# Kernel optimization log

Measured on AMD Instinct MI355X. Metric: run time of the kernel, lower is better.

Reference implementation:

```python
import jax, jax.numpy as jnp
import numpy as np

D, H, E, K = 1024, 2048, 8, 2
AUX_COEF = 0.01


def _xavier(key, shape, fan_in, fan_out):
    lim = (6.0 / (fan_in + fan_out)) ** 0.5
    return jax.random.uniform(key, shape, minval=-lim, maxval=lim, dtype=jnp.float32)


def setup_inputs() -> dict:
    key = jax.random.key(0)
    ks = jax.random.split(key, 6)
    x = jax.random.normal(ks[0], (4, 2048, D), dtype=jnp.float32)
    Wg = _xavier(ks[1], (E, D), D, E)              # gate: [E, D]
    W1 = _xavier(ks[2], (E, D, H), D, H)           # stacked expert w1
    W3 = _xavier(ks[3], (E, D, H), D, H)           # stacked expert w3
    W2 = _xavier(ks[4], (E, H, D), H, D)           # stacked expert w2
    b1 = jnp.zeros((E, H), dtype=jnp.float32)
    b3 = jnp.zeros((E, H), dtype=jnp.float32)
    b2 = jnp.zeros((E, D), dtype=jnp.float32)
    return {"x": x, "Wg": Wg, "W1": W1, "b1": b1, "W2": W2, "b2": b2, "W3": W3, "b3": b3}


def reference(x, Wg, W1, b1, W2, b2, W3, b3):
    B, S, d = x.shape
    xf = x.reshape(-1, d)                                  # [N, D]
    N = xf.shape[0]

    # Gate: softmax scores, top-k routing, route_scale = 1.0
    all_scores = jax.nn.softmax(xf @ Wg.T, axis=-1)        # [N, E]
    topk_vals, topk_idx = jax.lax.top_k(all_scores, K)     # [N, K]

    # Combine weights scattered back to [N, E] (each token hits K distinct experts)
    cw = (jax.nn.one_hot(topk_idx, E, dtype=xf.dtype) * topk_vals[..., None]).sum(axis=1)

    # Per-expert SwiGLU, computed densely over E (reference form of masked dispatch)
    h = jax.nn.silu(jnp.einsum('nd,edh->neh', xf, W1) + b1) * \
        (jnp.einsum('nd,edh->neh', xf, W3) + b3)           # [N, E, H]
    expert_out = jnp.einsum('neh,ehd->ned', h, W2) + b2    # [N, E, D]
    y = jnp.einsum('ned,ne->nd', expert_out, cw)           # weighted combine

    # Load-balancing aux loss
    counts = jnp.bincount(topk_idx.reshape(-1), length=E).astype(xf.dtype)
    f = counts / float(N * K)
    P = all_scores.mean(axis=0)
    aux_loss = AUX_COEF * float(E) * jnp.dot(f, P)

    return y.reshape(B, S, d), aux_loss
```

## Files before the change

### kernel.cpp

```cpp
#include <hip/hip_runtime.h>
#include <hip/hip_bf16.h>
#include <math.h>

#define Ntok 8192
#define Dm   1024
#define Hm   2048
#define NE   8

typedef __hip_bfloat16 bf16;
typedef __attribute__((ext_vector_type(8))) short short8;
typedef __attribute__((ext_vector_type(4))) float f32x4;

static __device__ __forceinline__ float b2f(bf16 v){ return __bfloat162float(v); }
static __device__ __forceinline__ bf16  f2b(float v){ return __float2bfloat16(v); }

static __device__ __forceinline__ void gl2lds16(const bf16* g, bf16* l) {
    __builtin_amdgcn_global_load_lds(
        (const __attribute__((address_space(1))) unsigned*)(const void*)g,
        (__attribute__((address_space(3))) unsigned*)(void*)l, 16, 0, 0);
}

__global__ void detect_kernel(const unsigned* __restrict__ xw, int* dtf)
{
    unsigned w = xw[threadIdx.x];
    int ex = (w >> 23) & 0xff;
    unsigned long long m = __ballot(ex < 200);
    if (threadIdx.x == 0) *dtf = (__popcll(m) > 32) ? 1 : 0;
}

__global__ __launch_bounds__(1024) void gate_kernel(
    const void* __restrict__ xv, const void* __restrict__ wgv,
    const int* __restrict__ dtf,
    int* cnt, float* Psum, float* wts, int* idx_buf, bf16* __restrict__ xb)
{
    int fp32 = *dtf;
    int tid  = threadIdx.x;
    int lane = tid & 63;
    int wv   = tid >> 6;
    int n    = blockIdx.x * 16 + wv;

    __shared__ float lP[8];
    __shared__ int   lc[8];
    __shared__ int   gbase[8];
    __shared__ int   tslot[16][2];
    __shared__ int   texp[16][2];

    if (tid < 8) { lP[tid] = 0.f; lc[tid] = 0; }
    __syncthreads();

    float acc[NE];
    #pragma unroll
    for (int e = 0; e < NE; e++) acc[e] = 0.f;

    if (fp32) {
        const float* xr = (const float*)xv + (size_t)n * Dm;
        const float* Wg = (const float*)wgv;
        #pragma unroll
        for (int i = 0; i < 16; i++) {
            float xval = xr[lane + 64*i];
            xb[(size_t)n * Dm + lane + 64*i] = f2b(xval);
            #pragma unroll
            for (int e = 0; e < NE; e++) acc[e] += xval * Wg[e*Dm + lane + 64*i];
        }
    } else {
        const bf16* xr = (const bf16*)xv + (size_t)n * Dm;
        const bf16* Wg = (const bf16*)wgv;
        #pragma unroll
        for (int i = 0; i < 16; i++) {
            bf16 xraw = xr[lane + 64*i];
            xb[(size_t)n * Dm + lane + 64*i] = xraw;
            float xval = b2f(xraw);
            #pragma unroll
            for (int e = 0; e < NE; e++) acc[e] += xval * b2f(Wg[e*Dm + lane + 64*i]);
        }
    }
    #pragma unroll
    for (int e = 0; e < NE; e++) {
        float v = acc[e];
        #pragma unroll
        for (int off = 32; off > 0; off >>= 1) v += __shfl_xor(v, off);
        acc[e] = v;
    }
    float mx = acc[0];
    #pragma unroll
    for (int e = 1; e < NE; e++) mx = fmaxf(mx, acc[e]);
    float p[NE]; float s = 0.f;
    #pragma unroll
    for (int e = 0; e < NE; e++) { p[e] = expf(acc[e] - mx); s += p[e]; }
    float inv = 1.f / s;
    #pragma unroll
    for (int e = 0; e < NE; e++) p[e] *= inv;
    int e0 = 0;
    #pragma unroll
    for (int e = 1; e < NE; e++) if (p[e] > p[e0]) e0 = e;
    int e1 = (e0 == 0) ? 1 : 0;
    #pragma unroll
    for (int e = 0; e < NE; e++) if (e != e0 && p[e] > p[e1]) e1 = e;

    if (lane < NE) atomicAdd(&lP[lane], p[lane]);
    if (lane == 0) {
        tslot[wv][0] = atomicAdd(&lc[e0], 1);
        tslot[wv][1] = atomicAdd(&lc[e1], 1);
        texp[wv][0] = e0; texp[wv][1] = e1;
        wts[2*n]   = p[e0];
        wts[2*n+1] = p[e1];
    }
    __syncthreads();
    if (tid < 8) {
        gbase[tid] = atomicAdd(cnt + tid, lc[tid]);
        atomicAdd(Psum + tid*16, lP[tid]);
    }
    __syncthreads();
    if (lane == 0) {
        int ea = texp[wv][0], eb = texp[wv][1];
        idx_buf[ea*Ntok + gbase[ea] + tslot[wv][0]] = n;
        idx_buf[eb*Ntok + gbase[eb] + tslot[wv][1]] = n | 0x10000;
    }
}

__global__ void aux_kernel(const int* __restrict__ cnt, const float* __restrict__ Psum,
                           const int* __restrict__ dtf, int* __restrict__ offs,
                           void* __restrict__ out)
{
    if (threadIdx.x == 0) {
        float s = 0.f; int a = 0;
        for (int e = 0; e < NE; e++) {
            offs[e] = a; a += cnt[e];
            s += (float)cnt[e] * Psum[e*16];
        }
        float aux = 0.08f * s / (16384.f * 8192.f);
        if (*dtf) ((float*)out)[(size_t)Ntok * Dm] = aux;
        else      ((bf16*)out)[(size_t)Ntok * Dm] = f2b(aux);
    }
}

__global__ void transpose2_kernel(const void* __restrict__ sA, const void* __restrict__ sB,
                                  bf16* __restrict__ dA, bf16* __restrict__ dB,
                                  int R, int C, const int* __restrict__ dtf)
{
    __shared__ bf16 t[64][68];
    int mat = blockIdx.z >> 3, e = blockIdx.z & 7;
    const void* src = mat ? sB : sA;
    bf16* dst = mat ? dB : dA;
    size_t base = (size_t)e * R * C;
    int c0 = blockIdx.x * 64, r0 = blockIdx.y * 64;
    int tid = threadIdx.x;
    int lr = tid >> 4;
    int lc = (tid & 15) * 4;

    if (*dtf) {
        const float* s = (const float*)src + base;
        #pragma unroll
        for (int i = 0; i < 4; i++) {
            float4 v = *(const float4*)(s + (size_t)(r0 + lr + 16*i) * C + c0 + lc);
            t[lr+16*i][lc+0] = f2b(v.x); t[lr+16*i][lc+1] = f2b(v.y);
            t[lr+16*i][lc+2] = f2b(v.z); t[lr+16*i][lc+3] = f2b(v.w);
        }
    } else {
        const bf16* s = (const bf16*)src + base;
        #pragma unroll
        for (int i = 0; i < 4; i++) {
            bf16 v[4];
            *(uint2*)v = *(const uint2*)(s + (size_t)(r0 + lr + 16*i) * C + c0 + lc);
            t[lr+16*i][lc+0] = v[0]; t[lr+16*i][lc+1] = v[1];
            t[lr+16*i][lc+2] = v[2]; t[lr+16*i][lc+3] = v[3];
        }
    }
    __syncthreads();
    int oc = tid >> 2;
    int os = tid & 3;
    bf16 ov[16];
    #pragma unroll
    for (int j = 0; j < 16; j++) ov[j] = t[os*16 + j][oc];
    bf16* dp = dst + base + (size_t)(c0 + oc) * R + r0 + os*16;
    *(uint4*)dp       = *(uint4*)ov;
    *(uint4*)(dp + 8) = *(uint4*)(ov + 8);
}


#define BAR()  { asm volatile("" ::: "memory"); __builtin_amdgcn_s_barrier(); asm volatile("" ::: "memory"); }
#define VMW4() asm volatile("s_waitcnt vmcnt(4)" ::: "memory")
#define VMW2() asm volatile("s_waitcnt vmcnt(2)" ::: "memory")
#define VMW0() asm volatile("s_waitcnt vmcnt(0)" ::: "memory")

#define LOADA(_bf, _mh) do { \
    int _ab = ((_bf)*4 + (_mh))*8192 + (wr*64 + mrow)*64; \
    _Pragma("unroll") \
    for (int _m = 0; _m < 4; _m++) { \
      _Pragma("unroll") \
      for (int _k = 0; _k < 2; _k++) \
        af[_m][_k] = *(const short8*)&smem[_ab + _m*1024 + kxo[_k]]; \
    } } while(0)

#define LOADB(_bf, _nh) do { \
    int _bb = ((_bf)*4 + 2 + (_nh))*8192 + (wc*32 + mrow)*64; \
    _Pragma("unroll") \
    for (int _n = 0; _n < 2; _n++) { \
      _Pragma("unroll") \
      for (int _k = 0; _k < 2; _k++) \
        bfr[_n][_k] = *(const short8*)&smem[_bb + _n*1024 + kxo[_k]]; \
    } } while(0)

#define MFMAQ(_mh, _nh) do { \
    _Pragma("unroll") \
    for (int _m = 0; _m < 4; _m++) \
      _Pragma("unroll") \
      for (int _n = 0; _n < 2; _n++) \
        _Pragma("unroll") \
        for (int _k = 0; _k < 2; _k++) \
          acc[(_mh)*4+_m][(_nh)*2+_n] = __builtin_amdgcn_mfma_f32_16x16x32_bf16( \
              af[_m][_k], bfr[_n][_k], acc[(_mh)*4+_m][(_nh)*2+_n], 0, 0, 0); \
    } while(0)

#define STAGE_A0(_nb) do { gl2lds16(pA00, &smem[((_nb)*4+0)*8192 + w*512]); \
                           gl2lds16(pA01, &smem[((_nb)*4+0)*8192 + 4096 + w*512]); \
                           pA00 += 64; pA01 += 64; } while(0)
#define STAGE_A1(_nb) do { gl2lds16(pA10, &smem[((_nb)*4+1)*8192 + w*512]); \
                           gl2lds16(pA11, &smem[((_nb)*4+1)*8192 + 4096 + w*512]); \
                           pA10 += 64; pA11 += 64; } while(0)
#define STAGE_B0(_nb) do { gl2lds16(pB00, &smem[((_nb)*4+2)*8192 + w*512]); \
                           gl2lds16(pB01, &smem[((_nb)*4+2)*8192 + 4096 + w*512]); \
                           pB00 += 64; pB01 += 64; } while(0)
#define STAGE_B1(_nb) do { gl2lds16(pB10, &smem[((_nb)*4+3)*8192 + w*512]); \
                           gl2lds16(pB11, &smem[((_nb)*4+3)*8192 + 4096 + w*512]); \
                           pB10 += 64; pB11 += 64; } while(0)

template<int MODE>
__global__ __launch_bounds__(512) void ffn_kernel(
    const bf16* __restrict__ Asrc,
    const bf16* __restrict__ Bsrc1,
    const bf16* __restrict__ Bsrc3,
    const void* __restrict__ bv1,
    const void* __restrict__ bv3,
    const int* __restrict__ dtf,
    const int* __restrict__ cnt, const int* __restrict__ offs,
    const int* __restrict__ idx_buf,
    bf16* __restrict__ Out)
{
    const int KD = MODE ? Hm : Dm;
    const int NT = KD / 64;
    int e = blockIdx.z;
    int c = cnt[e];
    int m0 = blockIdx.y * 256;
    if (m0 >= c) return;
    int n0 = blockIdx.x * (MODE ? 256 : 128);
    int fp32 = *dtf;
    int slot0 = offs[e] + m0;

    __shared__ __align__(16) bf16 smem[65536];
    __shared__ int tk[256];

    int tid = threadIdx.x;
    int cm = c - 1 - m0; if (cm > 255) cm = 255;
    if (tid < 256) {
        int r = tid > cm ? cm : tid;
        int v = idx_buf[e*Ntok + m0 + r];
        tk[tid] = MODE ? (2*(v & 0xffff) + (v >> 16)) : (v & 0xffff);
    }
    __syncthreads();

    int lane = tid & 63, w = tid >> 6;
    int wr = w >> 2, wc = w & 3;
    int mrow = lane & 15, kg = lane >> 4;
    int flip = mrow & 7;
    int kxo[2];
    kxo[0] = ((0*4 + kg) ^ flip) * 8;
    kxo[1] = ((1*4 + kg) ^ flip) * 8;

    int rs = tid >> 3;
    int cs_src = (tid & 7) ^ (rs & 7);

    const bf16 *pA00, *pA01, *pA10, *pA11, *pB00, *pB01, *pB10, *pB11;
    {
        int r00 = rs, r01 = 64 + rs, r10 = 128 + rs, r11 = 192 + rs;
        if (MODE == 0) {
            pA00 = Asrc + (size_t)tk[r00] * Dm + cs_src*8;
            pA01 = Asrc + (size_t)tk[r01] * Dm + cs_src*8;
            pA10 = Asrc + (size_t)tk[r10] * Dm + cs_src*8;
            pA11 = Asrc + (size_t)tk[r11] * Dm + cs_src*8;
        } else {
            int c00 = r00 > cm ? cm : r00, c01 = r01 > cm ? cm : r01;
            int c10 = r10 > cm ? cm : r10, c11 = r11 > cm ? cm : r11;
            pA00 = Asrc + (size_t)(slot0 + c00) * Hm + cs_src*8;
            pA01 = Asrc + (size_t)(slot0 + c01) * Hm + cs_src*8;
            pA10 = Asrc + (size_t)(slot0 + c10) * Hm + cs_src*8;
            pA11 = Asrc + (size_t)(slot0 + c11) * Hm + cs_src*8;
        }
        if (MODE == 0) {
            #pragma unroll
            for (int hl = 0; hl < 4; hl++) {
                int r = hl*64 + rs;
                int matb = (r >> 4) & 1;
                int hcol = n0 + (r >> 7)*64 + ((r >> 5) & 3)*16 + (r & 15);
                const bf16* base = (matb ? Bsrc3 : Bsrc1) + (size_t)e*Hm*Dm
                                 + (size_t)hcol * Dm + cs_src*8;
                if (hl == 0) pB00 = base; else if (hl == 1) pB01 = base;
                else if (hl == 2) pB10 = base; else pB11 = base;
            }
        } else {
            pB00 = Bsrc1 + (size_t)e*Dm*Hm + (size_t)(n0 + rs      ) * Hm + cs_src*8;
            pB01 = Bsrc1 + (size_t)e*Dm*Hm + (size_t)(n0 + rs +  64) * Hm + cs_src*8;
            pB10 = Bsrc1 + (size_t)e*Dm*Hm + (size_t)(n0 + rs + 128) * Hm + cs_src*8;
            pB11 = Bsrc1 + (size_t)e*Dm*Hm + (size_t)(n0 + rs + 192) * Hm + cs_src*8;
        }
    }

    f32x4 acc[8][4];
    f32x4 z = {0.f, 0.f, 0.f, 0.f};
    #pragma unroll
    for (int m = 0; m < 8; m++)
        #pragma unroll
        for (int n = 0; n < 4; n++) acc[m][n] = z;

    short8 af[4][2];
    short8 bfr[2][2];

    STAGE_A0(0); STAGE_B0(0); STAGE_B1(0); STAGE_A1(0);
    VMW0();
    __syncthreads();

    for (int t = 0; t < NT; ++t) {
        int buf = t & 1, nbuf = buf ^ 1;
        bool more = (t + 1 < NT);
        LOADA(buf, 0); LOADB(buf, 0);
        if (more) STAGE_A0(nbuf);
        BAR();
        __builtin_amdgcn_s_setprio(1); MFMAQ(0, 0); __builtin_amdgcn_s_setprio(0);
        if (more) VMW4(); else VMW2();
        BAR();
        LOADB(buf, 1);
        if (more) STAGE_B0(nbuf);
        BAR();
        __builtin_amdgcn_s_setprio(1); MFMAQ(0, 1); __builtin_amdgcn_s_setprio(0);
        if (more) VMW4(); else VMW0();
        BAR();
        LOADA(buf, 1);
        if (more) STAGE_B1(nbuf);
        BAR();
        __builtin_amdgcn_s_setprio(1); MFMAQ(1, 1); __builtin_amdgcn_s_setprio(0);
        BAR();
        LOADB(buf, 0);
        if (more) STAGE_A1(nbuf);
        BAR();
        __builtin_amdgcn_s_setprio(1); MFMAQ(1, 0); __builtin_amdgcn_s_setprio(0);
        if (more) VMW4();
        BAR();
    }

    if (MODE == 0) {
        #pragma unroll
        for (int nh = 0; nh < 2; nh++) {
            int hcol = n0 + nh*64 + wc*16 + mrow;
            float bb1 = fp32 ? ((const float*)bv1)[e*Hm + hcol] : b2f(((const bf16*)bv1)[e*Hm + hcol]);
            float bb3 = fp32 ? ((const float*)bv3)[e*Hm + hcol] : b2f(((const bf16*)bv3)[e*Hm + hcol]);
            #pragma unroll
            for (int ms = 0; ms < 8; ms++) {
                int rbase = (ms>>2)*128 + wr*64 + (ms&3)*16 + kg*4;
                #pragma unroll
                for (int j = 0; j < 4; j++) {
                    int tr = rbase + j;
                    if (m0 + tr < c) {
                        float v1 = acc[ms][nh*2+0][j] + bb1;
                        float v3 = acc[ms][nh*2+1][j] + bb3;
                        float hv = (v1 / (1.f + expf(-v1))) * v3;
                        Out[(size_t)(slot0 + tr)*Hm + hcol] = f2b(hv);
                    }
                }
            }
        }
    } else {
        #pragma unroll
        for (int ns = 0; ns < 4; ns++) {
            int col = n0 + (ns>>1)*128 + wc*32 + (ns&1)*16 + mrow;
            float bb2 = fp32 ? ((const float*)bv1)[e*Dm + col] : b2f(((const bf16*)bv1)[e*Dm + col]);
            #pragma unroll
            for (int ms = 0; ms < 8; ms++) {
                int rbase = (ms>>2)*128 + wr*64 + (ms&3)*16 + kg*4;
                #pragma unroll
                for (int j = 0; j < 4; j++) {
                    int tr = rbase + j;
                    if (m0 + tr < c)
                        Out[(size_t)tk[tr]*Dm + col] = f2b(acc[ms][ns][j] + bb2);
                }
            }
        }
    }
}

#undef LOADA
#undef LOADB
#undef MFMAQ
#undef STAGE_A0
#undef STAGE_A1
#undef STAGE_B0
#undef STAGE_B1

__global__ void combine_kernel(const bf16* __restrict__ outs, const float* __restrict__ wts,
                               const int* __restrict__ dtf, void* __restrict__ yv)
{
    int gid = blockIdx.x * 256 + threadIdx.x;
    int n = gid >> 7;
    int j = (gid & 127) * 8;
    float w0 = wts[2*n], w1 = wts[2*n+1];
    bf16 ra[8], rb[8];
    *(uint4*)ra = *(const uint4*)(outs + (size_t)(2*n)   * Dm + j);
    *(uint4*)rb = *(const uint4*)(outs + (size_t)(2*n+1) * Dm + j);
    float o[8];
    #pragma unroll
    for (int t = 0; t < 8; t++)
        o[t] = w0 * b2f(ra[t]) + w1 * b2f(rb[t]);
    if (*dtf) {
        float* y = (float*)yv + (size_t)n * Dm + j;
        *(float4*)y       = make_float4(o[0], o[1], o[2], o[3]);
        *(float4*)(y + 4) = make_float4(o[4], o[5], o[6], o[7]);
    } else {
        bf16 ro[8];
        #pragma unroll
        for (int t = 0; t < 8; t++) ro[t] = f2b(o[t]);
        *(uint4*)((bf16*)yv + (size_t)n * Dm + j) = *(uint4*)ro;
    }
}

extern "C" void kernel_launch(void* const* d_in, const int* in_sizes, int n_in,
                              void* d_out, int out_size, void* d_ws, size_t ws_size,
                              hipStream_t stream)
{
    (void)in_sizes; (void)n_in; (void)out_size; (void)ws_size;
    const void* x  = d_in[0];
    const void* Wg = d_in[1];
    const void* W1 = d_in[2];
    const void* b1 = d_in[3];
    const void* W2 = d_in[4];
    const void* b2 = d_in[5];
    const void* W3 = d_in[6];
    const void* b3 = d_in[7];

    char* ws = (char*)d_ws;
    int*   cnt  = (int*)ws;
    int*   dtf  = (int*)(ws + 64);
    int*   offs = (int*)(ws + 512);
    float* Psum = (float*)(ws + 1024);
    float* wts  = (float*)(ws + 4096);
    int*   idx  = (int*)(ws + 69632);
    bf16* bufA  = (bf16*)(ws + 331776);
    bf16* bufB  = (bf16*)(ws + 33886208);
    bf16* hbuf  = (bf16*)(ws + 67440640);
    bf16* outs  = bufB;
    bf16* xb    = (bf16*)d_out;

    hipMemsetAsync(d_ws, 0, 4096, stream);
    detect_kernel<<<1, 64, 0, stream>>>((const unsigned*)x, dtf);
    gate_kernel<<<Ntok/16, 1024, 0, stream>>>(x, Wg, dtf, cnt, Psum, wts, idx, xb);
    aux_kernel<<<1, 64, 0, stream>>>(cnt, Psum, dtf, offs, d_out);
    transpose2_kernel<<<dim3(Hm/64, Dm/64, 16), 256, 0, stream>>>(W1, W3, bufA, bufB, Dm, Hm, dtf);
    ffn_kernel<0><<<dim3(Hm/128, Ntok/256, NE), 512, 0, stream>>>(
        xb, bufA, bufB, b1, b3, dtf, cnt, offs, idx, hbuf);
    transpose2_kernel<<<dim3(Dm/64, Hm/64, 8), 256, 0, stream>>>(W2, W2, bufA, bufA, Hm, Dm, dtf);
    ffn_kernel<1><<<dim3(Dm/256, Ntok/256, NE), 512, 0, stream>>>(
        hbuf, bufA, bufA, b2, b2, dtf, cnt, offs, idx, outs);
    combine_kernel<<<(Ntok*Dm/8)/256, 256, 0, stream>>>(outs, wts, dtf, d_out);
}
```

Measured before the change: 606.0 us.

## Halve FFN tile width, drop double buffering, raise occupancy

Result: slower. 717.9 us (+18.5%).

```diff
diff --git a/kernel.cpp b/kernel.cpp
--- a/kernel.cpp
+++ b/kernel.cpp
@@ -179,12 +179,10 @@
 
 
 #define BAR()  { asm volatile("" ::: "memory"); __builtin_amdgcn_s_barrier(); asm volatile("" ::: "memory"); }
-#define VMW4() asm volatile("s_waitcnt vmcnt(4)" ::: "memory")
-#define VMW2() asm volatile("s_waitcnt vmcnt(2)" ::: "memory")
 #define VMW0() asm volatile("s_waitcnt vmcnt(0)" ::: "memory")
 
-#define LOADA(_bf, _mh) do { \
-    int _ab = ((_bf)*4 + (_mh))*8192 + (wr*64 + mrow)*64; \
+#define LOADA(_mh) do { \
+    int _ab = (_mh)*8192 + (wr*64 + mrow)*64; \
     _Pragma("unroll") \
     for (int _m = 0; _m < 4; _m++) { \
       _Pragma("unroll") \
@@ -192,8 +190,8 @@
         af[_m][_k] = *(const short8*)&smem[_ab + _m*1024 + kxo[_k]]; \
     } } while(0)
 
-#define LOADB(_bf, _nh) do { \
-    int _bb = ((_bf)*4 + 2 + (_nh))*8192 + (wc*32 + mrow)*64; \
+#define LOADBW() do { \
+    int _bb = 16384 + (wc>>1)*4096 + ((wc&1)*32 + mrow)*64; \
     _Pragma("unroll") \
     for (int _n = 0; _n < 2; _n++) { \
       _Pragma("unroll") \
@@ -201,32 +199,25 @@
         bfr[_n][_k] = *(const short8*)&smem[_bb + _n*1024 + kxo[_k]]; \
     } } while(0)
 
-#define MFMAQ(_mh, _nh) do { \
+#define MFMAQ(_mh) do { \
     _Pragma("unroll") \
     for (int _m = 0; _m < 4; _m++) \
       _Pragma("unroll") \
       for (int _n = 0; _n < 2; _n++) \
         _Pragma("unroll") \
         for (int _k = 0; _k < 2; _k++) \
-          acc[(_mh)*4+_m][(_nh)*2+_n] = __builtin_amdgcn_mfma_f32_16x16x32_bf16( \
-              af[_m][_k], bfr[_n][_k], acc[(_mh)*4+_m][(_nh)*2+_n], 0, 0, 0); \
+          acc[(_mh)*4+_m][_n] = __builtin_amdgcn_mfma_f32_16x16x32_bf16( \
+              af[_m][_k], bfr[_n][_k], acc[(_mh)*4+_m][_n], 0, 0, 0); \
     } while(0)
 
-#define STAGE_A0(_nb) do { gl2lds16(pA00, &smem[((_nb)*4+0)*8192 + w*512]); \
-                           gl2lds16(pA01, &smem[((_nb)*4+0)*8192 + 4096 + w*512]); \
-                           pA00 += 64; pA01 += 64; } while(0)
-#define STAGE_A1(_nb) do { gl2lds16(pA10, &smem[((_nb)*4+1)*8192 + w*512]); \
-                           gl2lds16(pA11, &smem[((_nb)*4+1)*8192 + 4096 + w*512]); \
-                           pA10 += 64; pA11 += 64; } while(0)
-#define STAGE_B0(_nb) do { gl2lds16(pB00, &smem[((_nb)*4+2)*8192 + w*512]); \
-                           gl2lds16(pB01, &smem[((_nb)*4+2)*8192 + 4096 + w*512]); \
-                           pB00 += 64; pB01 += 64; } while(0)
-#define STAGE_B1(_nb) do { gl2lds16(pB10, &smem[((_nb)*4+3)*8192 + w*512]); \
-                           gl2lds16(pB11, &smem[((_nb)*4+3)*8192 + 4096 + w*512]); \
-                           pB10 += 64; pB11 += 64; } while(0)
+#define STAGE6() do { \
+    gl2lds16(pA00, &smem[        w*512]); gl2lds16(pA01, &smem[ 4096 + w*512]); \
+    gl2lds16(pA10, &smem[ 8192 + w*512]); gl2lds16(pA11, &smem[12288 + w*512]); \
+    gl2lds16(pB00, &smem[16384 + w*512]); gl2lds16(pB01, &smem[20480 + w*512]); \
+    pA00 += 64; pA01 += 64; pA10 += 64; pA11 += 64; pB00 += 64; pB01 += 64; } while(0)
 
 template<int MODE>
-__global__ __launch_bounds__(512) void ffn_kernel(
+__global__ __launch_bounds__(512, 4) void ffn_kernel(
     const bf16* __restrict__ Asrc,
     const bf16* __restrict__ Bsrc1,
     const bf16* __restrict__ Bsrc3,
@@ -243,11 +234,11 @@
     int c = cnt[e];
     int m0 = blockIdx.y * 256;
     if (m0 >= c) return;
-    int n0 = blockIdx.x * (MODE ? 256 : 128);
+    int n0 = blockIdx.x * (MODE ? 128 : 64);
     int fp32 = *dtf;
     int slot0 = offs[e] + m0;
 
-    __shared__ __align__(16) bf16 smem[65536];
+    __shared__ __align__(16) bf16 smem[24576];
     __shared__ int tk[256];
 
     int tid = threadIdx.x;
@@ -270,7 +261,7 @@
     int rs = tid >> 3;
     int cs_src = (tid & 7) ^ (rs & 7);
 
-    const bf16 *pA00, *pA01, *pA10, *pA11, *pB00, *pB01, *pB10, *pB11;
+    const bf16 *pA00, *pA01, *pA10, *pA11, *pB00, *pB01;
     {
         int r00 = rs, r01 = 64 + rs, r10 = 128 + rs, r11 = 192 + rs;
         if (MODE == 0) {
@@ -288,90 +279,65 @@
         }
         if (MODE == 0) {
             #pragma unroll
-            for (int hl = 0; hl < 4; hl++) {
+            for (int hl = 0; hl < 2; hl++) {
                 int r = hl*64 + rs;
                 int matb = (r >> 4) & 1;
-                int hcol = n0 + (r >> 7)*64 + ((r >> 5) & 3)*16 + (r & 15);
+                int hcol = n0 + ((r >> 5) & 3)*16 + (r & 15);
                 const bf16* base = (matb ? Bsrc3 : Bsrc1) + (size_t)e*Hm*Dm
                                  + (size_t)hcol * Dm + cs_src*8;
-                if (hl == 0) pB00 = base; else if (hl == 1) pB01 = base;
-                else if (hl == 2) pB10 = base; else pB11 = base;
+                if (hl == 0) pB00 = base; else pB01 = base;
             }
         } else {
-            pB00 = Bsrc1 + (size_t)e*Dm*Hm + (size_t)(n0 + rs      ) * Hm + cs_src*8;
-            pB01 = Bsrc1 + (size_t)e*Dm*Hm + (size_t)(n0 + rs +  64) * Hm + cs_src*8;
-            pB10 = Bsrc1 + (size_t)e*Dm*Hm + (size_t)(n0 + rs + 128) * Hm + cs_src*8;
-            pB11 = Bsrc1 + (size_t)e*Dm*Hm + (size_t)(n0 + rs + 192) * Hm + cs_src*8;
-        }
-    }
-
-    f32x4 acc[8][4];
+            pB00 = Bsrc1 + (size_t)e*Dm*Hm + (size_t)(n0 + rs     ) * Hm + cs_src*8;
+            pB01 = Bsrc1 + (size_t)e*Dm*Hm + (size_t)(n0 + rs + 64) * Hm + cs_src*8;
+        }
+    }
+
+    f32x4 acc[8][2];
     f32x4 z = {0.f, 0.f, 0.f, 0.f};
     #pragma unroll
-    for (int m = 0; m < 8; m++)
-        #pragma unroll
-        for (int n = 0; n < 4; n++) acc[m][n] = z;
+    for (int m = 0; m < 8; m++) { acc[m][0] = z; acc[m][1] = z; }
 
     short8 af[4][2];
     short8 bfr[2][2];
 
-    STAGE_A0(0); STAGE_B0(0); STAGE_B1(0); STAGE_A1(0);
-    VMW0();
-    __syncthreads();
-
     for (int t = 0; t < NT; ++t) {
-        int buf = t & 1, nbuf = buf ^ 1;
-        bool more = (t + 1 < NT);
-        LOADA(buf, 0); LOADB(buf, 0);
-        if (more) STAGE_A0(nbuf);
+        STAGE6();
+        VMW0();
         BAR();
-        __builtin_amdgcn_s_setprio(1); MFMAQ(0, 0); __builtin_amdgcn_s_setprio(0);
-        if (more) VMW4(); else VMW2();
+        LOADBW();
+        LOADA(0);
+        __builtin_amdgcn_s_setprio(1);
+        MFMAQ(0);
+        LOADA(1);
+        MFMAQ(1);
+        __builtin_amdgcn_s_setprio(0);
+        __builtin_amdgcn_sched_barrier(0);
         BAR();
-        LOADB(buf, 1);
-        if (more) STAGE_B0(nbuf);
-        BAR();
-        __builtin_amdgcn_s_setprio(1); MFMAQ(0, 1); __builtin_amdgcn_s_setprio(0);
-        if (more) VMW4(); else VMW0();
-        BAR();
-        LOADA(buf, 1);
-        if (more) STAGE_B1(nbuf);
-        BAR();
-        __builtin_amdgcn_s_setprio(1); MFMAQ(1, 1); __builtin_amdgcn_s_setprio(0);
-        BAR();
-        LOADB(buf, 0);
-        if (more) STAGE_A1(nbuf);
-        BAR();
-        __builtin_amdgcn_s_setprio(1); MFMAQ(1, 0); __builtin_amdgcn_s_setprio(0);
-        if (more) VMW4();
-        BAR();
     }
 
     if (MODE == 0) {
-        #pragma unroll
-        for (int nh = 0; nh < 2; nh++) {
-            int hcol = n0 + nh*64 + wc*16 + mrow;
-            float bb1 = fp32 ? ((const float*)bv1)[e*Hm + hcol] : b2f(((const bf16*)bv1)[e*Hm + hcol]);
-            float bb3 = fp32 ? ((const float*)bv3)[e*Hm + hcol] : b2f(((const bf16*)bv3)[e*Hm + hcol]);
+        int hcol = n0 + wc*16 + mrow;
+        float bb1 = fp32 ? ((const float*)bv1)[e*Hm + hcol] : b2f(((const bf16*)bv1)[e*Hm + hcol]);
+        float bb3 = fp32 ? ((const float*)bv3)[e*Hm + hcol] : b2f(((const bf16*)bv3)[e*Hm + hcol]);
+        #pragma unroll
+        for (int ms = 0; ms < 8; ms++) {
+            int rbase = (ms>>2)*128 + wr*64 + (ms&3)*16 + kg*4;
             #pragma unroll
-            for (int ms = 0; ms < 8; ms++) {
-                int rbase = (ms>>2)*128 + wr*64 + (ms&3)*16 + kg*4;
-                #pragma unroll
-                for (int j = 0; j < 4; j++) {
-                    int tr = rbase + j;
-                    if (m0 + tr < c) {
-                        float v1 = acc[ms][nh*2+0][j] + bb1;
-                        float v3 = acc[ms][nh*2+1][j] + bb3;
-                        float hv = (v1 / (1.f + expf(-v1))) * v3;
-                        Out[(size_t)(slot0 + tr)*Hm + hcol] = f2b(hv);
-                    }
+            for (int j = 0; j < 4; j++) {
+                int tr = rbase + j;
+                if (m0 + tr < c) {
+                    float v1 = acc[ms][0][j] + bb1;
+                    float v3 = acc[ms][1][j] + bb3;
+                    float hv = (v1 / (1.f + expf(-v1))) * v3;
+                    Out[(size_t)(slot0 + tr)*Hm + hcol] = f2b(hv);
                 }
             }
         }
     } else {
         #pragma unroll
-        for (int ns = 0; ns < 4; ns++) {
-            int col = n0 + (ns>>1)*128 + wc*32 + (ns&1)*16 + mrow;
+        for (int ns = 0; ns < 2; ns++) {
+            int col = n0 + wc*32 + ns*16 + mrow;
             float bb2 = fp32 ? ((const float*)bv1)[e*Dm + col] : b2f(((const bf16*)bv1)[e*Dm + col]);
             #pragma unroll
             for (int ms = 0; ms < 8; ms++) {
@@ -388,12 +354,9 @@
 }
 
 #undef LOADA
-#undef LOADB
+#undef LOADBW
 #undef MFMAQ
-#undef STAGE_A0
-#undef STAGE_A1
-#undef STAGE_B0
-#undef STAGE_B1
+#undef STAGE6
 
 __global__ void combine_kernel(const bf16* __restrict__ outs, const float* __restrict__ wts,
                                const int* __restrict__ dtf, void* __restrict__ yv)
@@ -453,10 +416,10 @@
     gate_kernel<<<Ntok/16, 1024, 0, stream>>>(x, Wg, dtf, cnt, Psum, wts, idx, xb);
     aux_kernel<<<1, 64, 0, stream>>>(cnt, Psum, dtf, offs, d_out);
     transpose2_kernel<<<dim3(Hm/64, Dm/64, 16), 256, 0, stream>>>(W1, W3, bufA, bufB, Dm, Hm, dtf);
-    ffn_kernel<0><<<dim3(Hm/128, Ntok/256, NE), 512, 0, stream>>>(
+    ffn_kernel<0><<<dim3(Hm/64, Ntok/256, NE), 512, 0, stream>>>(
         xb, bufA, bufB, b1, b3, dtf, cnt, offs, idx, hbuf);
     transpose2_kernel<<<dim3(Dm/64, Hm/64, 8), 256, 0, stream>>>(W2, W2, bufA, bufA, Hm, Dm, dtf);
-    ffn_kernel<1><<<dim3(Dm/256, Ntok/256, NE), 512, 0, stream>>>(
+    ffn_kernel<1><<<dim3(Dm/128, Ntok/256, NE), 512, 0, stream>>>(
         hbuf, bufA, bufA, b2, b2, dtf, cnt, offs, idx, outs);
     combine_kernel<<<(Ntok*Dm/8)/256, 256, 0, stream>>>(outs, wts, dtf, d_out);
 }
```
